# Kernel optimization log

Hardware: AMD Instinct MI355X
Metric: run time of the kernel (lower is better)

The kernel has to match this reference:

```python
import jax, jax.numpy as jnp
import numpy as np

N = 4096
IN_F = 256
F = 64      # out_features
H = 4       # heads
NEG_SLOPE = 0.2


def setup_inputs() -> dict:
    key = jax.random.key(0)
    k1, k2, k3, k4 = jax.random.split(key, 4)
    x = jax.random.normal(k1, (N, IN_F), dtype=jnp.float32)
    # symmetric random binary adjacency with self-loops (avoids empty softmax rows)
    adj = jax.random.bernoulli(k2, 0.5, (N, N)).astype(jnp.float32)
    adj = jnp.clip(adj + adj.T, 0.0, 1.0)
    adj = jnp.maximum(adj, jnp.eye(N, dtype=jnp.float32))
    W = jax.random.normal(k3, (IN_F, F * H), dtype=jnp.float32) * (1.0 / np.sqrt(IN_F))
    a = jax.random.normal(k4, (2 * F, 1), dtype=jnp.float32) * 0.1
    return {"x": x, "adj": adj, "W": W, "a": a}


def reference(x, adj, W, a):
    # h: [N, H, F]
    h = (x @ W).reshape(N, H, F)
    # e[i, j, h] = leakyrelu(a_l . h[i, h] + a_r . h[j, h])  -- avoids the O(N^2*H*2F) concat
    a_l = a[:F, 0]
    a_r = a[F:, 0]
    el = jnp.einsum('nhf,f->nh', h, a_l)  # [N, H]
    er = jnp.einsum('nhf,f->nh', h, a_r)  # [N, H]
    e = jax.nn.leaky_relu(el[:, None, :] + er[None, :, :], NEG_SLOPE)  # [N, N, H]
    e = jnp.where(adj[:, :, None] == 0, -jnp.inf, e)
    attention = jax.nn.softmax(e, axis=1)  # softmax over neighbors j
    h_prime = jnp.einsum('ijh,jhf->ihf', attention, h)  # [N, H, F]
    return h_prime.mean(axis=1)  # [N, F]  (heads > 1 -> mean over heads)
```

## Files before the change

kernel.cpp:

```cpp
#include <hip/hip_runtime.h>
#include <hip/hip_bf16.h>

#define NN 4096
#define LOG2E 1.44269504088896340736f
#define SPLITS 8

typedef __attribute__((ext_vector_type(8))) short s8v;
typedef __attribute__((ext_vector_type(4))) float f4v;

__device__ __forceinline__ unsigned fu(float x){ union{float f;unsigned u;}z; z.f=x; return z.u; }
__device__ __forceinline__ unsigned pack2(float a, float b){
  return __builtin_amdgcn_perm(fu(b), fu(a), 0x07060302u);
}
__device__ __forceinline__ unsigned short f2bf_rne(float x){
  unsigned u = fu(x);
  u += 0x7fffu + ((u >> 16) & 1u);
  return (unsigned short)(u >> 16);
}

__global__ __launch_bounds__(256) void k1_proj(
    const float* __restrict__ x, const float* __restrict__ W,
    const float* __restrict__ a, unsigned short* __restrict__ Vt,
    float* __restrict__ el4, float* __restrict__ erT)
{
  __shared__ float4 xs[512];
  const int t = threadIdx.x;
  const int r0 = blockIdx.x * 8;
  const float4* xg = (const float4*)(x + (size_t)r0 * 256);
  xs[t] = xg[t];
  xs[t + 256] = xg[t + 256];
  __syncthreads();

  float acc[8] = {0.f,0.f,0.f,0.f,0.f,0.f,0.f,0.f};
  const float* Wp = W + t;
  #pragma unroll 2
  for (int k4 = 0; k4 < 64; ++k4) {
    float w0 = Wp[(k4*4+0)*256];
    float w1 = Wp[(k4*4+1)*256];
    float w2 = Wp[(k4*4+2)*256];
    float w3 = Wp[(k4*4+3)*256];
    #pragma unroll
    for (int r = 0; r < 8; ++r) {
      float4 xv = xs[r*64 + k4];
      acc[r] = fmaf(xv.x, w0, acc[r]);
      acc[r] = fmaf(xv.y, w1, acc[r]);
      acc[r] = fmaf(xv.z, w2, acc[r]);
      acc[r] = fmaf(xv.w, w3, acc[r]);
    }
  }

  union { unsigned u[4]; s8v v; } pk;
  #pragma unroll
  for (int p = 0; p < 4; ++p)
    pk.u[p] = (unsigned)f2bf_rne(acc[2*p]) | ((unsigned)f2bf_rne(acc[2*p+1]) << 16);
  *(s8v*)(Vt + (size_t)t * NN + r0) = pk.v;

  const int f = t & 63, h = t >> 6;
  const float al = a[f], ar = a[64 + f];
  #pragma unroll
  for (int r = 0; r < 8; ++r) {
    float v = acc[r] * al;
    float u = acc[r] * ar;
    #pragma unroll
    for (int off = 32; off > 0; off >>= 1) {
      v += __shfl_xor(v, off);
      u += __shfl_xor(u, off);
    }
    if (f == 0) {
      el4[(r0 + r) * 4 + h] = v * LOG2E;
      erT[h * NN + (r0 + r)] = u * LOG2E;
    }
  }
}

__global__ __launch_bounds__(256, 2) void k2_attn(
    const float* __restrict__ adj, const unsigned short* __restrict__ Vt,
    const float* __restrict__ el4, const float* __restrict__ erT,
    float* __restrict__ accP, float* __restrict__ lP)
{
  const int t = threadIdx.x;
  const int w = t >> 6, l = t & 63;
  const int m = l & 15, q = l >> 4;
  const int i0 = blockIdx.x * 64;
  const int split = blockIdx.y;
  const int i = i0 + w * 16 + m;

  float4 elv4 = *(const float4*)(el4 + i * 4);
  float elv[4] = {elv4.x, elv4.y, elv4.z, elv4.w};

  f4v acc[4][4];
  #pragma unroll
  for (int h = 0; h < 4; ++h)
    #pragma unroll
    for (int nf = 0; nf < 4; ++nf)
      acc[h][nf] = (f4v){0.f, 0.f, 0.f, 0.f};
  float lsum[4] = {0.f, 0.f, 0.f, 0.f};

  const float* arow = adj + (size_t)i * NN;
  int j0 = split * 512 + q * 8;

  #pragma unroll 1
  for (int jc = 0; jc < 16; ++jc, j0 += 32) {
    float4 a0 = *(const float4*)(arow + j0);
    float4 a1 = *(const float4*)(arow + j0 + 4);
    #pragma unroll
    for (int h = 0; h < 4; ++h) {
      float4 e0 = *(const float4*)(erT + h * NN + j0);
      float4 e1 = *(const float4*)(erT + h * NN + j0 + 4);
      const float eh = elv[h];
      float t0 = eh + e0.x, t1 = eh + e0.y, t2 = eh + e0.z, t3 = eh + e0.w;
      float t4 = eh + e1.x, t5 = eh + e1.y, t6 = eh + e1.z, t7 = eh + e1.w;
      float s0 = a0.x * __builtin_amdgcn_exp2f(fmaxf(t0, 0.2f*t0));
      float s1 = a0.y * __builtin_amdgcn_exp2f(fmaxf(t1, 0.2f*t1));
      float s2 = a0.z * __builtin_amdgcn_exp2f(fmaxf(t2, 0.2f*t2));
      float s3 = a0.w * __builtin_amdgcn_exp2f(fmaxf(t3, 0.2f*t3));
      float s4 = a1.x * __builtin_amdgcn_exp2f(fmaxf(t4, 0.2f*t4));
      float s5 = a1.y * __builtin_amdgcn_exp2f(fmaxf(t5, 0.2f*t5));
      float s6 = a1.z * __builtin_amdgcn_exp2f(fmaxf(t6, 0.2f*t6));
      float s7 = a1.w * __builtin_amdgcn_exp2f(fmaxf(t7, 0.2f*t7));
      lsum[h] += ((s0+s1)+(s2+s3)) + ((s4+s5)+(s6+s7));
      union { unsigned u[4]; s8v v; } A;
      A.u[0] = pack2(s0, s1);
      A.u[1] = pack2(s2, s3);
      A.u[2] = pack2(s4, s5);
      A.u[3] = pack2(s6, s7);
      const unsigned short* vb = Vt + (size_t)(h * 64 + m) * NN + j0;
      #pragma unroll
      for (int nf = 0; nf < 4; ++nf) {
        s8v B = *(const s8v*)(vb + (size_t)nf * 16 * NN);
        acc[h][nf] = __builtin_amdgcn_mfma_f32_16x16x32_bf16(A.v, B, acc[h][nf], 0, 0, 0);
      }
    }
  }

  #pragma unroll
  for (int h = 0; h < 4; ++h) {
    float v = lsum[h];
    v += __shfl_xor(v, 16);
    v += __shfl_xor(v, 32);
    lsum[h] = v;
  }
  if (l < 16) {
    int row = i0 + w * 16 + l;
    float4 lv = make_float4(lsum[0], lsum[1], lsum[2], lsum[3]);
    *(float4*)(lP + ((size_t)split * NN + row) * 4) = lv;
  }
  float* ap = accP + (size_t)split * NN * 256;
  #pragma unroll
  for (int h = 0; h < 4; ++h)
    #pragma unroll
    for (int nf = 0; nf < 4; ++nf)
      #pragma unroll
      for (int r = 0; r < 4; ++r) {
        int row = i0 + w * 16 + q * 4 + r;
        int col = h * 64 + nf * 16 + m;
        ap[(size_t)row * 256 + col] = acc[h][nf][r];
      }
}

__global__ __launch_bounds__(256) void k3_reduce(
    const float* __restrict__ accP, const float* __restrict__ lP,
    float* __restrict__ out)
{
  int tid = blockIdx.x * 256 + threadIdx.x;
  int i = tid >> 6, f = tid & 63;
  float o = 0.f;
  #pragma unroll
  for (int h = 0; h < 4; ++h) {
    float sa = 0.f, sl = 0.f;
    #pragma unroll
    for (int s = 0; s < SPLITS; ++s) {
      sa += accP[((size_t)s * NN + i) * 256 + h * 64 + f];
      sl += lP[((size_t)s * NN + i) * 4 + h];
    }
    o += sa / sl;
  }
  out[tid] = 0.25f * o;
}

extern "C" void kernel_launch(void* const* d_in, const int* in_sizes, int n_in,
                              void* d_out, int out_size, void* d_ws, size_t ws_size,
                              hipStream_t stream) {
  const float* x   = (const float*)d_in[0];
  const float* adj = (const float*)d_in[1];
  const float* W   = (const float*)d_in[2];
  const float* a   = (const float*)d_in[3];
  float* out = (float*)d_out;

  char* ws = (char*)d_ws;
  unsigned short* Vt = (unsigned short*)ws;
  float* el4 = (float*)(ws + (2u << 20));
  float* erT = (float*)(ws + (2u << 20) + (64u << 10));
  float* lP  = (float*)(ws + (2u << 20) + (128u << 10));
  float* accP= (float*)(ws + (2u << 20) + (128u << 10) + (512u << 10));

  k1_proj<<<512, 256, 0, stream>>>(x, W, a, Vt, el4, erT);
  k2_attn<<<dim3(64, SPLITS), 256, 0, stream>>>(adj, Vt, el4, erT, accP, lP);
  k3_reduce<<<1024, 256, 0, stream>>>(accP, lP, out);
}
```

Baseline: 190.6 us.

## Factor exp of leaky-relu logits, split heads across waves, MFMA row sums

Removes the per-pair exp2 by rewriting exp2(leakyrelu(el+er)) as max(2^el*2^er, 2^(0.2el)*2^(0.2er)), with the per-node exponentials computed once in the projection kernel. Each wave now handles two heads for 16 rows, so blocks cover 32 rows, the grid doubles and occupancy is raised to 4 blocks per SM. Row sums move from VALU adds and shuffles into an extra MFMA against a ones vector, and the next adjacency chunk is prefetched. The factored form uses no max-subtraction, so large logits could overflow fp32, and twice as many blocks now reread the same Vt tiles.

```diff
diff --git a/kernel.cpp b/kernel.cpp
--- a/kernel.cpp
+++ b/kernel.cpp
@@ -21,7 +21,7 @@
 __global__ __launch_bounds__(256) void k1_proj(
     const float* __restrict__ x, const float* __restrict__ W,
     const float* __restrict__ a, unsigned short* __restrict__ Vt,
-    float* __restrict__ el4, float* __restrict__ erT)
+    float* __restrict__ el4, float* __restrict__ Qr, float* __restrict__ Sr)
 {
   __shared__ float4 xs[512];
   const int t = threadIdx.x;
@@ -68,57 +68,75 @@
     }
     if (f == 0) {
       el4[(r0 + r) * 4 + h] = v * LOG2E;
-      erT[h * NN + (r0 + r)] = u * LOG2E;
-    }
-  }
-}
-
-__global__ __launch_bounds__(256, 2) void k2_attn(
+      float up = u * LOG2E;
+      Qr[h * NN + (r0 + r)] = __builtin_amdgcn_exp2f(up);
+      Sr[h * NN + (r0 + r)] = __builtin_amdgcn_exp2f(0.2f * up);
+    }
+  }
+}
+
+__global__ __launch_bounds__(256, 4) void k2_attn(
     const float* __restrict__ adj, const unsigned short* __restrict__ Vt,
-    const float* __restrict__ el4, const float* __restrict__ erT,
-    float* __restrict__ accP, float* __restrict__ lP)
+    const float* __restrict__ el4, const float* __restrict__ Qr,
+    const float* __restrict__ Sr, float* __restrict__ accP,
+    float* __restrict__ lP)
 {
   const int t = threadIdx.x;
   const int w = t >> 6, l = t & 63;
   const int m = l & 15, q = l >> 4;
-  const int i0 = blockIdx.x * 64;
+  const int rw = w & 1, hw = w >> 1;
+  const int i0 = blockIdx.x * 32;
   const int split = blockIdx.y;
-  const int i = i0 + w * 16 + m;
-
-  float4 elv4 = *(const float4*)(el4 + i * 4);
-  float elv[4] = {elv4.x, elv4.y, elv4.z, elv4.w};
-
-  f4v acc[4][4];
-  #pragma unroll
-  for (int h = 0; h < 4; ++h)
+  const int i = i0 + rw * 16 + m;
+  const int h0 = hw * 2;
+
+  const float el0 = el4[i * 4 + h0];
+  const float el1 = el4[i * 4 + h0 + 1];
+  const float P[2] = { __builtin_amdgcn_exp2f(el0), __builtin_amdgcn_exp2f(el1) };
+  const float R[2] = { __builtin_amdgcn_exp2f(0.2f * el0), __builtin_amdgcn_exp2f(0.2f * el1) };
+
+  f4v acc[2][4];
+  #pragma unroll
+  for (int hh = 0; hh < 2; ++hh)
     #pragma unroll
     for (int nf = 0; nf < 4; ++nf)
-      acc[h][nf] = (f4v){0.f, 0.f, 0.f, 0.f};
-  float lsum[4] = {0.f, 0.f, 0.f, 0.f};
+      acc[hh][nf] = (f4v){0.f, 0.f, 0.f, 0.f};
+  f4v accL[2] = { (f4v){0.f,0.f,0.f,0.f}, (f4v){0.f,0.f,0.f,0.f} };
+
+  union { unsigned u[4]; s8v v; } ones;
+  #pragma unroll
+  for (int p = 0; p < 4; ++p) ones.u[p] = 0x3F803F80u;
 
   const float* arow = adj + (size_t)i * NN;
   int j0 = split * 512 + q * 8;
 
+  float4 a0 = *(const float4*)(arow + j0);
+  float4 a1 = *(const float4*)(arow + j0 + 4);
+
   #pragma unroll 1
-  for (int jc = 0; jc < 16; ++jc, j0 += 32) {
-    float4 a0 = *(const float4*)(arow + j0);
-    float4 a1 = *(const float4*)(arow + j0 + 4);
-    #pragma unroll
-    for (int h = 0; h < 4; ++h) {
-      float4 e0 = *(const float4*)(erT + h * NN + j0);
-      float4 e1 = *(const float4*)(erT + h * NN + j0 + 4);
-      const float eh = elv[h];
-      float t0 = eh + e0.x, t1 = eh + e0.y, t2 = eh + e0.z, t3 = eh + e0.w;
-      float t4 = eh + e1.x, t5 = eh + e1.y, t6 = eh + e1.z, t7 = eh + e1.w;
-      float s0 = a0.x * __builtin_amdgcn_exp2f(fmaxf(t0, 0.2f*t0));
-      float s1 = a0.y * __builtin_amdgcn_exp2f(fmaxf(t1, 0.2f*t1));
-      float s2 = a0.z * __builtin_amdgcn_exp2f(fmaxf(t2, 0.2f*t2));
-      float s3 = a0.w * __builtin_amdgcn_exp2f(fmaxf(t3, 0.2f*t3));
-      float s4 = a1.x * __builtin_amdgcn_exp2f(fmaxf(t4, 0.2f*t4));
-      float s5 = a1.y * __builtin_amdgcn_exp2f(fmaxf(t5, 0.2f*t5));
-      float s6 = a1.z * __builtin_amdgcn_exp2f(fmaxf(t6, 0.2f*t6));
-      float s7 = a1.w * __builtin_amdgcn_exp2f(fmaxf(t7, 0.2f*t7));
-      lsum[h] += ((s0+s1)+(s2+s3)) + ((s4+s5)+(s6+s7));
+  for (int jc = 0; jc < 16; ++jc) {
+    const int jn = (jc < 15) ? (j0 + 32) : j0;
+    float4 na0 = *(const float4*)(arow + jn);
+    float4 na1 = *(const float4*)(arow + jn + 4);
+
+    #pragma unroll
+    for (int hh = 0; hh < 2; ++hh) {
+      const int h = h0 + hh;
+      const float* qp = Qr + h * NN + j0;
+      const float* sp = Sr + h * NN + j0;
+      float4 q0 = *(const float4*)(qp);
+      float4 q1 = *(const float4*)(qp + 4);
+      float4 sv0 = *(const float4*)(sp);
+      float4 sv1 = *(const float4*)(sp + 4);
+      const float Ph = P[hh], Rh = R[hh];
+      float s0 = a0.x * fmaxf(Ph * q0.x, Rh * sv0.x);
+      float s1 = a0.y * fmaxf(Ph * q0.y, Rh * sv0.y);
+      float s2 = a0.z * fmaxf(Ph * q0.z, Rh * sv0.z);
+      float s3 = a0.w * fmaxf(Ph * q0.w, Rh * sv0.w);
+      float s4 = a1.x * fmaxf(Ph * q1.x, Rh * sv1.x);
+      float s5 = a1.y * fmaxf(Ph * q1.y, Rh * sv1.y);
+      float s6 = a1.z * fmaxf(Ph * q1.z, Rh * sv1.z);
+      float s7 = a1.w * fmaxf(Ph * q1.w, Rh * sv1.w);
       union { unsigned u[4]; s8v v; } A;
       A.u[0] = pack2(s0, s1);
       A.u[1] = pack2(s2, s3);
@@ -128,34 +146,34 @@
       #pragma unroll
       for (int nf = 0; nf < 4; ++nf) {
         s8v B = *(const s8v*)(vb + (size_t)nf * 16 * NN);
-        acc[h][nf] = __builtin_amdgcn_mfma_f32_16x16x32_bf16(A.v, B, acc[h][nf], 0, 0, 0);
+        acc[hh][nf] = __builtin_amdgcn_mfma_f32_16x16x32_bf16(A.v, B, acc[hh][nf], 0, 0, 0);
       }
-    }
-  }
-
-  #pragma unroll
-  for (int h = 0; h < 4; ++h) {
-    float v = lsum[h];
-    v += __shfl_xor(v, 16);
-    v += __shfl_xor(v, 32);
-    lsum[h] = v;
-  }
-  if (l < 16) {
-    int row = i0 + w * 16 + l;
-    float4 lv = make_float4(lsum[0], lsum[1], lsum[2], lsum[3]);
-    *(float4*)(lP + ((size_t)split * NN + row) * 4) = lv;
-  }
+      accL[hh] = __builtin_amdgcn_mfma_f32_16x16x32_bf16(A.v, ones.v, accL[hh], 0, 0, 0);
+    }
+    j0 += 32;
+    a0 = na0; a1 = na1;
+  }
+
   float* ap = accP + (size_t)split * NN * 256;
   #pragma unroll
-  for (int h = 0; h < 4; ++h)
+  for (int hh = 0; hh < 2; ++hh)
     #pragma unroll
     for (int nf = 0; nf < 4; ++nf)
       #pragma unroll
       for (int r = 0; r < 4; ++r) {
-        int row = i0 + w * 16 + q * 4 + r;
-        int col = h * 64 + nf * 16 + m;
-        ap[(size_t)row * 256 + col] = acc[h][nf][r];
+        int row = i0 + rw * 16 + q * 4 + r;
+        int col = (h0 + hh) * 64 + nf * 16 + m;
+        ap[(size_t)row * 256 + col] = acc[hh][nf][r];
       }
+  if (m == 0) {
+    #pragma unroll
+    for (int hh = 0; hh < 2; ++hh)
+      #pragma unroll
+      for (int r = 0; r < 4; ++r) {
+        int row = i0 + rw * 16 + q * 4 + r;
+        lP[((size_t)split * NN + row) * 4 + h0 + hh] = accL[hh][r];
+      }
+  }
 }
 
 __global__ __launch_bounds__(256) void k3_reduce(
@@ -190,11 +208,12 @@
   char* ws = (char*)d_ws;
   unsigned short* Vt = (unsigned short*)ws;
   float* el4 = (float*)(ws + (2u << 20));
-  float* erT = (float*)(ws + (2u << 20) + (64u << 10));
-  float* lP  = (float*)(ws + (2u << 20) + (128u << 10));
-  float* accP= (float*)(ws + (2u << 20) + (128u << 10) + (512u << 10));
-
-  k1_proj<<<512, 256, 0, stream>>>(x, W, a, Vt, el4, erT);
-  k2_attn<<<dim3(64, SPLITS), 256, 0, stream>>>(adj, Vt, el4, erT, accP, lP);
+  float* Qr  = (float*)(ws + (2u << 20) + (64u << 10));
+  float* Sr  = (float*)(ws + (2u << 20) + (128u << 10));
+  float* lP  = (float*)(ws + (2u << 20) + (192u << 10));
+  float* accP= (float*)(ws + (2u << 20) + (192u << 10) + (512u << 10));
+
+  k1_proj<<<512, 256, 0, stream>>>(x, W, a, Vt, el4, Qr, Sr);
+  k2_attn<<<dim3(128, SPLITS), 256, 0, stream>>>(adj, Vt, el4, Qr, Sr, accP, lP);
   k3_reduce<<<1024, 256, 0, stream>>>(accP, lP, out);
 }
```

Result: slower. 216.6 us (+13.7%).
